# Performance work log

Measured on AMD Instinct MI355X. Metric: run time of the kernel, lower is better.

Reference implementation:

```python
import jax, jax.numpy as jnp
import numpy as np

B, D, S, U, H = 2, 1024, 2048, 1024, 16
LN_EPS = 1e-5

def setup_inputs() -> dict:
    key = jax.random.key(0)
    ks = jax.random.split(key, 5)
    std = 0.02
    return {
        "inputs": jax.random.normal(ks[0], (B, D, S), jnp.float32),
        "Wq": jax.random.normal(ks[1], (D, U), jnp.float32) * std,
        "bq": jnp.zeros((U,), jnp.float32),
        "Wk": jax.random.normal(ks[2], (D, U), jnp.float32) * std,
        "bk": jnp.zeros((U,), jnp.float32),
        "Wv": jax.random.normal(ks[3], (D, U), jnp.float32) * std,
        "bv": jnp.zeros((U,), jnp.float32),
        "Wo": jax.random.normal(ks[4], (U, D), jnp.float32) * std,
        "bo": jnp.zeros((D,), jnp.float32),
        "gamma": jnp.ones((D,), jnp.float32),
        "beta": jnp.zeros((D,), jnp.float32),
        "num_heads": H,
    }

def reference(inputs, Wq, bq, Wk, bk, Wv, bv, Wo, bo, gamma, beta, num_heads):
    # inputs: (B, D, S) -> (B, S, D)
    x = jnp.transpose(inputs, (0, 2, 1))
    b, s, d = x.shape

    def proj(W, bias):
        y = jax.nn.relu(x @ W + bias)               # (b, s, U)
        y = y.reshape(b, s, num_heads, -1)
        return jnp.transpose(y, (0, 2, 1, 3))       # (b, h, s, hd)

    Q = proj(Wq, bq)
    K = proj(Wk, bk)
    V = proj(Wv, bv)
    hd = Q.shape[-1]
    scale = 1.0 / np.sqrt(hd).astype(np.float32)

    # Block-wise flash attention in the source is mathematically plain softmax attention
    # (per-block epsilon 1e-10 is negligible); scale applied to Q, no mask, no dropout.
    scores = jnp.einsum('bhid,bhjd->bhij', Q * scale, K)   # (b, h, s, s)
    P = jax.nn.softmax(scores, axis=-1)
    O = jnp.einsum('bhij,bhjd->bhid', P, V)                # (b, h, s, hd)

    O = jnp.transpose(O, (0, 2, 1, 3)).reshape(b, s, -1)   # (b, s, U)
    out = O @ Wo + bo + x                                  # residual add
    mean = jnp.mean(out, axis=-1, keepdims=True)
    var = jnp.var(out, axis=-1, keepdims=True)
    y = (out - mean) * jax.lax.rsqrt(var + LN_EPS) * gamma + beta
    return jnp.transpose(y, (0, 2, 1))                     # (B, D, S)
```

## Files before the change

kernel.cpp:

```cpp
#include <hip/hip_runtime.h>
#include <hip/hip_bf16.h>

typedef __bf16 bf16x8 __attribute__((ext_vector_type(8)));
typedef __bf16 bf16x4 __attribute__((ext_vector_type(4)));
typedef float  f32x4  __attribute__((ext_vector_type(4)));
typedef float  f32x16 __attribute__((ext_vector_type(16)));

#define MFMA16(a, b, c) __builtin_amdgcn_mfma_f32_16x16x32_bf16((a), (b), (c), 0, 0, 0)
#define MFMA32(a, b, c) __builtin_amdgcn_mfma_f32_32x32x16_bf16((a), (b), (c), 0, 0, 0)

namespace {
constexpr int Bb = 2, Dd = 1024, Ss = 2048, Uu = 1024, Hh = 16;
}

#if __has_builtin(__builtin_amdgcn_exp2f)
#define EXP2(x) __builtin_amdgcn_exp2f(x)
#else
#define EXP2(x) __expf((x) * 0.6931471805599453f)
#endif

__device__ __forceinline__ uint32_t pkbf(float a, float b) {
  union { __bf16 h[2]; uint32_t u; } z;
  z.h[0] = (__bf16)a; z.h[1] = (__bf16)b;
  return z.u;
}
#define PLSWAP(a, b) asm("v_permlane32_swap_b32 %0, %1" : "+v"(a), "+v"(b))

__device__ __forceinline__ void gl16(const void* g, void* l) {
  __builtin_amdgcn_global_load_lds((const __attribute__((address_space(1))) uint32_t*)g,
                                   (__attribute__((address_space(3))) uint32_t*)l, 16, 0, 0);
}

#define VMW(n) asm volatile("s_waitcnt vmcnt(" #n ")" ::: "memory")
#define BARRIER_PIN() do { __builtin_amdgcn_s_barrier(); \
  asm volatile("" ::: "memory"); __builtin_amdgcn_sched_barrier(0); } while (0)
#define LGKM0() asm volatile("s_waitcnt lgkmcnt(0)" ::: "memory")

__global__ __launch_bounds__(256) void k_xpose_x(const float* __restrict__ inp,
                                                 __bf16* __restrict__ xb, float* __restrict__ xt) {
  __shared__ __attribute__((aligned(16))) float xs[64][65];
  const int s0 = blockIdx.x * 64, d0 = blockIdx.y * 64, b = blockIdx.z;
  const int t = threadIdx.x;
  {
    const int i = t >> 2, c = (t & 3) * 16;
    const float* src = inp + ((size_t)(b * Dd + d0 + i)) * Ss + s0 + c;
#pragma unroll
    for (int q = 0; q < 4; ++q) {
      const float4 f = *(const float4*)(src + q * 4);
      xs[i][c + q * 4 + 0] = f.x; xs[i][c + q * 4 + 1] = f.y;
      xs[i][c + q * 4 + 2] = f.z; xs[i][c + q * 4 + 3] = f.w;
    }
  }
  __syncthreads();
  {
    const int sl = t >> 2, dc = (t & 3) * 16;
    float* dstf = xt + ((size_t)(b * Ss + s0 + sl)) * Dd + d0 + dc;
    bf16x8 va, vb;
#pragma unroll
    for (int q = 0; q < 4; ++q) {
      float4 f;
      f.x = xs[dc + q * 4 + 0][sl]; f.y = xs[dc + q * 4 + 1][sl];
      f.z = xs[dc + q * 4 + 2][sl]; f.w = xs[dc + q * 4 + 3][sl];
      *(float4*)(dstf + q * 4) = f;
    }
#pragma unroll
    for (int j = 0; j < 8; ++j) { va[j] = (__bf16)xs[dc + j][sl]; vb[j] = (__bf16)xs[dc + 8 + j][sl]; }
    __bf16* dst = xb + ((size_t)(b * Ss + s0 + sl)) * Dd + d0 + dc;
    *(bf16x8*)dst = va;
    *(bf16x8*)(dst + 8) = vb;
  }
}

__global__ __launch_bounds__(256) void k_xpose_w(const float* __restrict__ w0, const float* __restrict__ w1,
                                                 const float* __restrict__ w2, const float* __restrict__ w3,
                                                 __bf16* __restrict__ o0, __bf16* __restrict__ o1,
                                                 __bf16* __restrict__ o2, __bf16* __restrict__ o3) {
  __shared__ __attribute__((aligned(16))) __bf16 ts[64][72];
  const float* src_m; __bf16* dst_m;
  switch (blockIdx.z) {
    case 0: src_m = w0; dst_m = o0; break;
    case 1: src_m = w1; dst_m = o1; break;
    case 2: src_m = w2; dst_m = o2; break;
    default: src_m = w3; dst_m = o3; break;
  }
  const int n0 = blockIdx.x * 64, k0 = blockIdx.y * 64;
  const int t = threadIdx.x;
  {
    const int i = t >> 2, c = (t & 3) * 16;
    const float* src = src_m + (size_t)(k0 + i) * 1024 + n0 + c;
#pragma unroll
    for (int q = 0; q < 4; ++q) {
      const float4 f = *(const float4*)(src + q * 4);
      ts[i][c + q * 4 + 0] = (__bf16)f.x;
      ts[i][c + q * 4 + 1] = (__bf16)f.y;
      ts[i][c + q * 4 + 2] = (__bf16)f.z;
      ts[i][c + q * 4 + 3] = (__bf16)f.w;
    }
  }
  __syncthreads();
  {
    const int nl = t >> 2, kc = (t & 3) * 16;
    bf16x8 va, vb;
#pragma unroll
    for (int j = 0; j < 8; ++j) { va[j] = ts[kc + j][nl]; vb[j] = ts[kc + 8 + j][nl]; }
    __bf16* dst = dst_m + (size_t)(n0 + nl) * 1024 + k0 + kc;
    *(bf16x8*)dst = va;
    *(bf16x8*)(dst + 8) = vb;
  }
}

__device__ __forceinline__ int swz_slot(int row, int slot) { return (slot + (row >> 1)) & 3; }

__device__ __forceinline__ void gemm_core(const __bf16* __restrict__ A, const __bf16* __restrict__ Bt,
                                          __bf16 (*__restrict__ As)[128][32], __bf16 (*__restrict__ Bs)[128][32],
                                          int m0, int n0, int t, f32x4 acc[4][4]) {
  const int w = t >> 6, l = t & 63;
  const int wm = (w >> 1) * 64, wn = (w & 1) * 64;
  const int lg = l >> 4, lr = l & 15;
  const int sr = t >> 2, sc8 = t & 3;
  const int so = ((sc8 + 4 - ((sr >> 1) & 3)) & 3) * 8;
  const __bf16* ga = A + (size_t)(m0 + sr) * 1024 + so;
  const __bf16* gb = Bt + (size_t)(n0 + sr) * 1024 + so;
  const int de = sr * 32 + sc8 * 8;
#define STG(bf, kk) { \
    gl16(ga + (kk) * 32,             &As[bf][0][0] + de); \
    gl16(ga + (kk) * 32 + 64 * 1024, &As[bf][0][0] + de + 64 * 32); \
    gl16(gb + (kk) * 32,             &Bs[bf][0][0] + de); \
    gl16(gb + (kk) * 32 + 64 * 1024, &Bs[bf][0][0] + de + 64 * 32); }
  STG(0, 0) STG(1, 1)
  for (int s = 0; s < 32; ++s) {
    if (s < 31) { VMW(4); } else { VMW(0); }
    BARRIER_PIN();
    if (s + 2 < 32) { const int b2 = (s + 2) % 3; STG(b2, s + 2) }
    const int cb = s % 3;
    bf16x8 af[4], bfr[4];
#pragma unroll
    for (int i = 0; i < 4; ++i) { const int rr = wm + i * 16 + lr; af[i]  = *(const bf16x8*)&As[cb][rr][swz_slot(rr, lg) * 8]; }
#pragma unroll
    for (int i = 0; i < 4; ++i) { const int rr = wn + i * 16 + lr; bfr[i] = *(const bf16x8*)&Bs[cb][rr][swz_slot(rr, lg) * 8]; }
#pragma unroll
    for (int i = 0; i < 4; ++i)
#pragma unroll
      for (int j = 0; j < 4; ++j) acc[i][j] = MFMA16(af[i], bfr[j], acc[i][j]);
  }
#undef STG
}

__device__ __forceinline__ void epi_qk_c(f32x4 acc[4][4], const float* bias, __bf16* out,
                                         int m0, int n0, int t, float scale, __bf16* Ct) {
  const int w = t >> 6, l = t & 63;
  const int wm = (w >> 1) * 64, wn = (w & 1) * 64;
  const int lg = l >> 4, lr = l & 15;
  __syncthreads();
#pragma unroll
  for (int j = 0; j < 4; ++j) {
    const int nl = wn + j * 16 + lr;
    const float bi = bias[n0 + nl];
#pragma unroll
    for (int i = 0; i < 4; ++i)
#pragma unroll
      for (int r = 0; r < 4; ++r) {
        const int ml = wm + i * 16 + lg * 4 + r;
        Ct[ml * 132 + nl] = (__bf16)(fmaxf(acc[i][j][r] + bi, 0.0f) * scale);
      }
  }
  __syncthreads();
  const int b = m0 >> 11, h0 = n0 >> 6, sb = m0 & 2047;
  const int sub = t & 7, rid0 = t >> 3;
#pragma unroll
  for (int p = 0; p < 8; ++p) {
    const int rid = p * 32 + rid0;
    const int sl = rid & 127, hh = rid >> 7;
    const bf16x8 v = *(const bf16x8*)&Ct[sl * 132 + hh * 64 + sub * 8];
    *(bf16x8*)(out + ((size_t)(b * Hh + h0 + hh) * Ss + sb + sl) * 64 + sub * 8) = v;
  }
}

__device__ __forceinline__ void epi_vt_c(f32x4 acc[4][4], const float* bias, __bf16* out,
                                         int m0, int n0, int t, __bf16* Ct) {
  const int w = t >> 6, l = t & 63;
  const int wm = (w >> 1) * 64, wn = (w & 1) * 64;
  const int lg = l >> 4, lr = l & 15;
  __syncthreads();
#pragma unroll
  for (int j = 0; j < 4; ++j) {
    const int nl = wn + j * 16 + lr;
    const float bi = bias[n0 + nl];
#pragma unroll
    for (int i = 0; i < 4; ++i)
#pragma unroll
      for (int r = 0; r < 4; ++r) {
        const int ml = wm + i * 16 + lg * 4 + r;
        Ct[nl * 132 + ml] = (__bf16)fmaxf(acc[i][j][r] + bi, 0.0f);
      }
  }
  __syncthreads();
  const int b = m0 >> 11, sb = m0 & 2047;
  const int sub = t & 15, rid0 = t >> 4;
#pragma unroll
  for (int p = 0; p < 8; ++p) {
    const int rid = p * 16 + rid0;
    const bf16x8 v = *(const bf16x8*)&Ct[rid * 132 + sub * 8];
    *(bf16x8*)(out + (size_t)(b * 1024 + n0 + rid) * Ss + sb + sub * 8) = v;
  }
}

__global__ __launch_bounds__(256) void k_gemm_qkv(const __bf16* __restrict__ A,
    const __bf16* __restrict__ W0, const __bf16* __restrict__ W1, const __bf16* __restrict__ W2,
    const float* __restrict__ b0, const float* __restrict__ b1, const float* __restrict__ b2,
    __bf16* __restrict__ Qb, __bf16* __restrict__ Kb, __bf16* __restrict__ Vt) {
  __shared__ __attribute__((aligned(16))) char smem[49152];
  auto As = (__bf16 (*)[128][32])smem;
  auto Bs = (__bf16 (*)[128][32])(smem + 24576);
  __bf16* Ct = (__bf16*)smem;
  const int flat = blockIdx.x;
  const int logical = (flat & 7) * 96 + (flat >> 3);
  const int z = logical >> 8;
  const int rem = logical & 255;
  const int n0 = (rem & 7) * 128, m0 = (rem >> 3) * 128;
  const __bf16* Bt = (z == 0) ? W0 : (z == 1) ? W1 : W2;
  const float* bias = (z == 0) ? b0 : (z == 1) ? b1 : b2;
  const int t = threadIdx.x;
  f32x4 acc[4][4] = {};
  gemm_core(A, Bt, As, Bs, m0, n0, t, acc);
  if (z == 0) epi_qk_c(acc, bias, Qb, m0, n0, t, 0.125f * 1.44269504f, Ct);
  else if (z == 1) epi_qk_c(acc, bias, Kb, m0, n0, t, 1.0f, Ct);
  else epi_vt_c(acc, bias, Vt, m0, n0, t, Ct);
}

__global__ __launch_bounds__(256) void k_gemm_o(const __bf16* __restrict__ A, const __bf16* __restrict__ Bt,
                                                const float* __restrict__ bias, const float* __restrict__ xt,
                                                float* __restrict__ Wb, float* __restrict__ partials) {
  __shared__ __attribute__((aligned(16))) char smem[49152];
  auto As = (__bf16 (*)[128][32])smem;
  auto Bs = (__bf16 (*)[128][32])(smem + 24576);
  float* Cs = (float*)smem;
  const int flat = blockIdx.x;
  const int logical = (flat & 7) * 32 + (flat >> 3);
  const int n0 = (logical & 7) * 128, m0 = (logical >> 3) * 128;
  const int t = threadIdx.x, w = t >> 6, l = t & 63;
  const int wm = (w >> 1) * 64, wn = (w & 1) * 64;
  const int lg = l >> 4, lr = l & 15;
  f32x4 acc[4][4] = {};
  gemm_core(A, Bt, As, Bs, m0, n0, t, acc);
  const int sub = t & 31, rid0 = t >> 5;
#pragma unroll
  for (int h2 = 0; h2 < 2; ++h2) {
    __syncthreads();
    if ((w >> 1) == h2) {
#pragma unroll
      for (int j = 0; j < 4; ++j) {
        const int nl = wn + j * 16 + lr;
        const float bi = bias[n0 + nl];
#pragma unroll
        for (int i = 0; i < 4; ++i)
#pragma unroll
          for (int r = 0; r < 4; ++r)
            Cs[(i * 16 + lg * 4 + r) * 132 + nl] = acc[i][j][r] + bi;
      }
    }
    __syncthreads();
#pragma unroll
    for (int p = 0; p < 8; ++p) {
      const int row = p * 8 + rid0;
      const int m = m0 + h2 * 64 + row;
      float4 v = *(const float4*)&Cs[row * 132 + sub * 4];
      const float4 x4 = *(const float4*)&xt[(size_t)m * 1024 + n0 + sub * 4];
      v.x += x4.x; v.y += x4.y; v.z += x4.z; v.w += x4.w;
      *(float4*)&Wb[(size_t)m * 1024 + n0 + sub * 4] = v;
      float s = v.x + v.y + v.z + v.w;
      float q = v.x * v.x + v.y * v.y + v.z * v.z + v.w * v.w;
      s += __shfl_xor(s, 1); s += __shfl_xor(s, 2); s += __shfl_xor(s, 4); s += __shfl_xor(s, 8);
      q += __shfl_xor(q, 1); q += __shfl_xor(q, 2); q += __shfl_xor(q, 4); q += __shfl_xor(q, 8);
      if ((sub & 15) == 0) {
        const int ci = (n0 >> 6) + (sub >> 4);
        partials[((size_t)m * 16 + ci) * 2]     = s;
        partials[((size_t)m * 16 + ci) * 2 + 1] = q;
      }
    }
  }
}

__global__ __launch_bounds__(256, 2) void k_attn6(const __bf16* __restrict__ Qg, const __bf16* __restrict__ Kg,
                                                  const __bf16* __restrict__ Vt, __bf16* __restrict__ Og) {
  __shared__ __attribute__((aligned(16))) char smem[36864];
  auto Ks = (__bf16 (*)[64][72])smem;
  auto Vs = (__bf16 (*)[64][72])(smem + 18432);
  __bf16* Os = (__bf16*)smem;
  const int t = threadIdx.x, l = t & 63, w = t >> 6;
  const int ln = l & 31, hi = l >> 5;
  const int bid = blockIdx.x;
  const int orig = (bid & 7) * 64 + (bid >> 3);
  const int bh = orig >> 4, qt = orig & 15;
  const int q0blk = qt * 128;
  const int q0w = q0blk + w * 32;
  const int b = bh >> 4, h = bh & 15;
  const size_t kbase = (size_t)bh * Ss * 64;
  const int srow = t >> 2, scol = (t & 3) * 16;
  const __bf16* Krow = Kg + kbase + (size_t)srow * 64 + scol;
  const __bf16* Vrow = Vt + (size_t)(bh * 64 + srow) * Ss + scol;

  bf16x8 qf0, qf1, qf2, qf3;
  {
    const __bf16* qp = Qg + kbase + (size_t)(q0w + ln) * 64 + hi * 8;
    qf0 = *(const bf16x8*)(qp);
    qf1 = *(const bf16x8*)(qp + 16);
    qf2 = *(const bf16x8*)(qp + 32);
    qf3 = *(const bf16x8*)(qp + 48);
  }
  f32x16 oA = {}, oB = {};
  float lrow = 0.f;

  auto tile_compute = [&](const __bf16 (&K)[64][72], const __bf16 (&V)[64][72]) {
    f32x16 s0 = {}, s1 = {};
    {
      bf16x8 kf;
#define QK(u, cc, sacc) \
      kf = *(const bf16x8*)&K[(u) * 32 + ln][(cc) * 16 + hi * 8]; \
      sacc = MFMA32(kf, qf##cc, sacc);
      QK(0, 0, s0) QK(0, 1, s0) QK(0, 2, s0) QK(0, 3, s0)
      QK(1, 0, s1) QK(1, 1, s1) QK(1, 2, s1) QK(1, 3, s1)
#undef QK
    }
#pragma unroll
    for (int r = 0; r < 16; ++r) s0[r] = EXP2(s0[r]);
#pragma unroll
    for (int r = 0; r < 16; ++r) s1[r] = EXP2(s1[r]);
    float sm[16];
#pragma unroll
    for (int r = 0; r < 8; ++r) sm[r] = s0[2 * r] + s0[2 * r + 1];
#pragma unroll
    for (int r = 0; r < 8; ++r) sm[8 + r] = s1[2 * r] + s1[2 * r + 1];
#pragma unroll
    for (int st = 8; st > 0; st >>= 1)
#pragma unroll
      for (int r = 0; r < st; ++r) sm[r] += sm[r + st];
    lrow += sm[0];
    uint32_t w0[8], w1[8];
#pragma unroll
    for (int k = 0; k < 8; ++k) w0[k] = pkbf(s0[2 * k], s0[2 * k + 1]);
#pragma unroll
    for (int k = 0; k < 8; ++k) w1[k] = pkbf(s1[2 * k], s1[2 * k + 1]);
    PLSWAP(w0[0], w0[2]); PLSWAP(w0[1], w0[3]);
    PLSWAP(w0[4], w0[6]); PLSWAP(w0[5], w0[7]);
    PLSWAP(w1[0], w1[2]); PLSWAP(w1[1], w1[3]);
    PLSWAP(w1[4], w1[6]); PLSWAP(w1[5], w1[7]);
    union U4 { uint32_t u[4]; bf16x8 v; };
    U4 z;
    bf16x8 pa0, pa1, pa2, pa3;
    z.u[0] = w0[0]; z.u[1] = w0[1]; z.u[2] = w0[2]; z.u[3] = w0[3]; pa0 = z.v;
    z.u[0] = w0[4]; z.u[1] = w0[5]; z.u[2] = w0[6]; z.u[3] = w0[7]; pa1 = z.v;
    z.u[0] = w1[0]; z.u[1] = w1[1]; z.u[2] = w1[2]; z.u[3] = w1[3]; pa2 = z.v;
    z.u[0] = w1[4]; z.u[1] = w1[5]; z.u[2] = w1[6]; z.u[3] = w1[7]; pa3 = z.v;
    {
      bf16x8 vf;
#define PV(half, ti, pa, oacc) \
      vf = *(const bf16x8*)&V[(half) * 32 + ln][(ti) * 16 + hi * 8]; \
      oacc = MFMA32(vf, pa, oacc);
      PV(0, 0, pa0, oA) PV(0, 1, pa1, oA) PV(0, 2, pa2, oA) PV(0, 3, pa3, oA)
      PV(1, 0, pa0, oB) PV(1, 1, pa1, oB) PV(1, 2, pa2, oB) PV(1, 3, pa3, oB)
#undef PV
    }
  };

  bf16x8 kA0 = *(const bf16x8*)(Krow),      kA1 = *(const bf16x8*)(Krow + 8);
  bf16x8 vA0 = *(const bf16x8*)(Vrow),      vA1 = *(const bf16x8*)(Vrow + 8);
  bf16x8 kB0 = *(const bf16x8*)(Krow + 64 * 64), kB1 = *(const bf16x8*)(Krow + 64 * 64 + 8);
  bf16x8 vB0 = *(const bf16x8*)(Vrow + 64), vB1 = *(const bf16x8*)(Vrow + 64 + 8);

  for (int tt = 0; tt < 16; ++tt) {
    *(bf16x8*)&Ks[0][srow][scol]     = kA0;
    *(bf16x8*)&Ks[0][srow][scol + 8] = kA1;
    *(bf16x8*)&Vs[0][srow][scol]     = vA0;
    *(bf16x8*)&Vs[0][srow][scol + 8] = vA1;
    LGKM0();
    BARRIER_PIN();
    if (tt < 15) {
      const size_t ko = (size_t)(2 * tt + 2) * 64;
      kA0 = *(const bf16x8*)(Krow + ko * 64);
      kA1 = *(const bf16x8*)(Krow + ko * 64 + 8);
      vA0 = *(const bf16x8*)(Vrow + ko);
      vA1 = *(const bf16x8*)(Vrow + ko + 8);
    }
    tile_compute(Ks[0], Vs[0]);
    *(bf16x8*)&Ks[1][srow][scol]     = kB0;
    *(bf16x8*)&Ks[1][srow][scol + 8] = kB1;
    *(bf16x8*)&Vs[1][srow][scol]     = vB0;
    *(bf16x8*)&Vs[1][srow][scol + 8] = vB1;
    LGKM0();
    BARRIER_PIN();
    if (tt < 15) {
      const size_t ko = (size_t)(2 * tt + 3) * 64;
      kB0 = *(const bf16x8*)(Krow + ko * 64);
      kB1 = *(const bf16x8*)(Krow + ko * 64 + 8);
      vB0 = *(const bf16x8*)(Vrow + ko);
      vB1 = *(const bf16x8*)(Vrow + ko + 8);
    }
    tile_compute(Ks[1], Vs[1]);
  }
  {
    uint32_t a = __builtin_bit_cast(uint32_t, lrow), bsw = a;
    PLSWAP(a, bsw);
    lrow = __builtin_bit_cast(float, a) + __builtin_bit_cast(float, bsw);
  }
  const float rl = 1.0f / lrow;
  __syncthreads();
  const int ql = w * 32 + ln;
#pragma unroll
  for (int r0 = 0; r0 < 4; ++r0)
#pragma unroll
    for (int j = 0; j < 4; ++j) {
      Os[ql * 68 + hi * 4 + r0 * 8 + j]      = (__bf16)(oA[r0 * 4 + j] * rl);
      Os[ql * 68 + 32 + hi * 4 + r0 * 8 + j] = (__bf16)(oB[r0 * 4 + j] * rl);
    }
  __syncthreads();
  const int sub = t & 7, rid0 = t >> 3;
#pragma unroll
  for (int p = 0; p < 4; ++p) {
    const int rid = p * 32 + rid0;
    const bf16x8 v = *(const bf16x8*)&Os[rid * 68 + sub * 8];
    *(bf16x8*)(Og + ((size_t)(b * Ss + q0blk + rid)) * Uu + h * 64 + sub * 8) = v;
  }
}

__global__ __launch_bounds__(256) void k_ln_stats(const float* __restrict__ partials, float* __restrict__ stats) {
  const int row = blockIdx.x * 256 + threadIdx.x;
  float s = 0.f, q = 0.f;
#pragma unroll
  for (int c = 0; c < 16; ++c) {
    s += partials[((size_t)row * 16 + c) * 2];
    q += partials[((size_t)row * 16 + c) * 2 + 1];
  }
  const float mean = s * (1.0f / 1024.0f);
  const float var = q * (1.0f / 1024.0f) - mean * mean;
  stats[row * 2] = mean;
  stats[row * 2 + 1] = rsqrtf(var + 1e-5f);
}

__global__ __launch_bounds__(256) void k_ln_write(const float* __restrict__ Wb, const float* __restrict__ stats,
                                                  const float* __restrict__ gamma, const float* __restrict__ beta,
                                                  float* __restrict__ out) {
  __shared__ __attribute__((aligned(16))) float ws0[64][65];
  __shared__ float sm[64][2];
  const int d0 = blockIdx.x * 64, s0 = blockIdx.y * 64, b = blockIdx.z;
  const int t = threadIdx.x;
  {
    const int sl = t >> 2, dc = (t & 3) * 16;
    const float* src = Wb + ((size_t)(b * Ss + s0 + sl)) * Dd + d0 + dc;
#pragma unroll
    for (int q = 0; q < 4; ++q) {
      const float4 f = *(const float4*)(src + q * 4);
      ws0[dc + q * 4 + 0][sl] = f.x; ws0[dc + q * 4 + 1][sl] = f.y;
      ws0[dc + q * 4 + 2][sl] = f.z; ws0[dc + q * 4 + 3][sl] = f.w;
    }
  }
  if (t < 128) sm[t >> 1][t & 1] = stats[(size_t)(b * Ss + s0 + (t >> 1)) * 2 + (t & 1)];
  __syncthreads();
  const int dl = t >> 2, sc = (t & 3) * 16;
  const float g = gamma[d0 + dl], be = beta[d0 + dl];
  float* dst = out + ((size_t)(b * Dd + d0 + dl)) * Ss + s0 + sc;
#pragma unroll
  for (int q = 0; q < 4; ++q) {
    float4 o;
    o.x = (ws0[dl][sc + q * 4 + 0] - sm[sc + q * 4 + 0][0]) * sm[sc + q * 4 + 0][1] * g + be;
    o.y = (ws0[dl][sc + q * 4 + 1] - sm[sc + q * 4 + 1][0]) * sm[sc + q * 4 + 1][1] * g + be;
    o.z = (ws0[dl][sc + q * 4 + 2] - sm[sc + q * 4 + 2][0]) * sm[sc + q * 4 + 2][1] * g + be;
    o.w = (ws0[dl][sc + q * 4 + 3] - sm[sc + q * 4 + 3][0]) * sm[sc + q * 4 + 3][1] * g + be;
    *(float4*)(dst + q * 4) = o;
  }
}

extern "C" void kernel_launch(void* const* d_in, const int* in_sizes, int n_in,
                              void* d_out, int out_size, void* d_ws, size_t ws_size,
                              hipStream_t stream) {
  const float* inp   = (const float*)d_in[0];
  const float* Wq    = (const float*)d_in[1];
  const float* bq    = (const float*)d_in[2];
  const float* Wk    = (const float*)d_in[3];
  const float* bk    = (const float*)d_in[4];
  const float* Wv    = (const float*)d_in[5];
  const float* bv    = (const float*)d_in[6];
  const float* Wo    = (const float*)d_in[7];
  const float* bo    = (const float*)d_in[8];
  const float* gamma = (const float*)d_in[9];
  const float* beta  = (const float*)d_in[10];

  char* ws = (char*)d_ws;
  const size_t MB = 1ull << 20;
  __bf16* xb  = (__bf16*)(ws);
  __bf16* Wqt = (__bf16*)(ws + 8 * MB);
  __bf16* Wkt = (__bf16*)(ws + 10 * MB);
  __bf16* Wvt = (__bf16*)(ws + 12 * MB);
  __bf16* Wot = (__bf16*)(ws + 14 * MB);
  __bf16* Qb  = (__bf16*)(ws + 16 * MB);
  __bf16* Kb  = (__bf16*)(ws + 24 * MB);
  __bf16* Vtb = (__bf16*)(ws + 32 * MB);
  __bf16* Ob  = (__bf16*)(ws + 40 * MB);
  float*  xt  = (float*)(ws + 48 * MB);
  float*  Wb  = (float*)(ws + 16 * MB);
  float*  partials = (float*)(ws + 8 * MB);
  float*  stats    = (float*)(ws + 8 * MB + 512 * 1024);

  k_xpose_x<<<dim3(32, 16, 2), 256, 0, stream>>>(inp, xb, xt);
  k_xpose_w<<<dim3(16, 16, 4), 256, 0, stream>>>(Wq, Wk, Wv, Wo, Wqt, Wkt, Wvt, Wot);
  k_gemm_qkv<<<dim3(768), 256, 0, stream>>>(xb, Wqt, Wkt, Wvt, bq, bk, bv, Qb, Kb, Vtb);
  k_attn6<<<dim3(512), 256, 0, stream>>>(Qb, Kb, Vtb, Ob);
  k_gemm_o<<<dim3(256), 256, 0, stream>>>(Ob, Wot, bo, xt, Wb, partials);
  k_ln_stats<<<dim3(16), 256, 0, stream>>>(partials, stats);
  k_ln_write<<<dim3(16, 32, 2), 256, 0, stream>>>(Wb, stats, gamma, beta, (float*)d_out);
}
```

Measured before the change: 145.4 us.

## Replace QKV GEMM with 256x256-tile, 8-wave, 4-stage pipelined kernel

The fused QKV projection GEMM now uses 256x256 output tiles with 512 threads (8 waves, each computing 128x64) instead of 128x128 tiles with 256 threads. It uses a 4-stage LDS ring with split A/B staging interleaved between two MFMA phases, setprio around MFMA bursts, and a chunked epilogue that writes Q/K head-major and V transposed via LDS. The aim is more operand reuse per LDS load and less global traffic per FLOP. In exchange the grid shrinks from 768 to 192 blocks, fewer than the CU count, and register and LDS pressure rise.

```diff
diff --git a/kernel.cpp b/kernel.cpp
--- a/kernel.cpp
+++ b/kernel.cpp
@@ -106,6 +106,147 @@
     __bf16* dst = dst_m + (size_t)(n0 + nl) * 1024 + k0 + kc;
     *(bf16x8*)dst = va;
     *(bf16x8*)(dst + 8) = vb;
+  }
+}
+
+__global__ __launch_bounds__(512, 2) void k_gemm_qkv8(const __bf16* __restrict__ A,
+    const __bf16* __restrict__ W0, const __bf16* __restrict__ W1, const __bf16* __restrict__ W2,
+    const float* __restrict__ b0, const float* __restrict__ b1, const float* __restrict__ b2,
+    __bf16* __restrict__ Qb, __bf16* __restrict__ Kb, __bf16* __restrict__ Vt) {
+  __shared__ __attribute__((aligned(16))) __bf16 As[4][256][32];
+  __shared__ __attribute__((aligned(16))) __bf16 Bs[4][256][32];
+  const int t = threadIdx.x;
+  const int w = t >> 6, l = t & 63, lg = l >> 4, lr = l & 15;
+  const int wm = w >> 2, wn = w & 3;
+  const int bid = blockIdx.x;
+  const int logical = (bid & 7) * 24 + (bid >> 3);
+  const int z = logical >> 6;
+  const int rem = logical & 63;
+  const int n0 = (rem & 3) * 256, m0 = (rem >> 2) * 256;
+  const __bf16* Bt = z == 0 ? W0 : z == 1 ? W1 : W2;
+  const float* bias = z == 0 ? b0 : z == 1 ? b1 : b2;
+
+  const int srow = t >> 2, scol = (t & 3) * 8;
+  const __bf16* gaB = A  + ((size_t)(m0 + srow)) * 1024 + scol;
+  const __bf16* gbB = Bt + ((size_t)(n0 + srow)) * 1024 + scol;
+#define STG_A(s, h, kt) gl16(gaB + (size_t)(h) * 128 * 1024 + (kt) * 32, &As[s][(h) * 128 + srow][scol])
+#define STG_B(s, h, kt) gl16(gbB + (size_t)(h) * 128 * 1024 + (kt) * 32, &Bs[s][(h) * 128 + srow][scol])
+
+  STG_A(0, 0, 0); STG_A(0, 1, 0); STG_B(0, 0, 0); STG_B(0, 1, 0);
+  STG_A(1, 0, 1); STG_A(1, 1, 1); STG_B(1, 0, 1); STG_B(1, 1, 1);
+  STG_A(2, 0, 2); STG_A(2, 1, 2); STG_B(2, 0, 2); STG_B(2, 1, 2);
+  f32x4 acc[8][4] = {};
+  VMW(8);
+  BARRIER_PIN();
+
+  const __bf16* Abase = &As[0][0][0] + wm * 4096 + lr * 32 + lg * 8;
+  const __bf16* Bbase = &Bs[0][0][0] + wn * 2048 + lr * 32 + lg * 8;
+
+  for (int kt = 0; kt < 32; ++kt) {
+    const int sC = kt & 3, sS = (kt + 3) & 3;
+    const __bf16* Ap = Abase + sC * 8192;
+    const __bf16* Bp = Bbase + sC * 8192;
+    bf16x8 a0, a1, a2, a3, bb0, bb1, bb2, bb3;
+    a0 = *(const bf16x8*)(Ap);         a1 = *(const bf16x8*)(Ap + 512);
+    a2 = *(const bf16x8*)(Ap + 1024);  a3 = *(const bf16x8*)(Ap + 1536);
+    bb0 = *(const bf16x8*)(Bp);        bb1 = *(const bf16x8*)(Bp + 512);
+    bb2 = *(const bf16x8*)(Bp + 1024); bb3 = *(const bf16x8*)(Bp + 1536);
+    if (kt < 29) { STG_A(sS, 0, kt + 3); STG_A(sS, 1, kt + 3); }
+    BARRIER_PIN();
+    LGKM0(); __builtin_amdgcn_sched_barrier(0);
+    __builtin_amdgcn_s_setprio(1);
+    acc[0][0] = MFMA16(a0, bb0, acc[0][0]); acc[0][1] = MFMA16(a0, bb1, acc[0][1]);
+    acc[0][2] = MFMA16(a0, bb2, acc[0][2]); acc[0][3] = MFMA16(a0, bb3, acc[0][3]);
+    acc[1][0] = MFMA16(a1, bb0, acc[1][0]); acc[1][1] = MFMA16(a1, bb1, acc[1][1]);
+    acc[1][2] = MFMA16(a1, bb2, acc[1][2]); acc[1][3] = MFMA16(a1, bb3, acc[1][3]);
+    acc[2][0] = MFMA16(a2, bb0, acc[2][0]); acc[2][1] = MFMA16(a2, bb1, acc[2][1]);
+    acc[2][2] = MFMA16(a2, bb2, acc[2][2]); acc[2][3] = MFMA16(a2, bb3, acc[2][3]);
+    acc[3][0] = MFMA16(a3, bb0, acc[3][0]); acc[3][1] = MFMA16(a3, bb1, acc[3][1]);
+    acc[3][2] = MFMA16(a3, bb2, acc[3][2]); acc[3][3] = MFMA16(a3, bb3, acc[3][3]);
+    __builtin_amdgcn_s_setprio(0);
+    BARRIER_PIN();
+    a0 = *(const bf16x8*)(Ap + 2048);  a1 = *(const bf16x8*)(Ap + 2560);
+    a2 = *(const bf16x8*)(Ap + 3072);  a3 = *(const bf16x8*)(Ap + 3584);
+    if (kt < 29) { STG_B(sS, 0, kt + 3); STG_B(sS, 1, kt + 3); }
+    if (kt < 29) { VMW(8); } else if (kt == 29) { VMW(4); } else if (kt == 30) { VMW(0); }
+    BARRIER_PIN();
+    LGKM0(); __builtin_amdgcn_sched_barrier(0);
+    __builtin_amdgcn_s_setprio(1);
+    acc[4][0] = MFMA16(a0, bb0, acc[4][0]); acc[4][1] = MFMA16(a0, bb1, acc[4][1]);
+    acc[4][2] = MFMA16(a0, bb2, acc[4][2]); acc[4][3] = MFMA16(a0, bb3, acc[4][3]);
+    acc[5][0] = MFMA16(a1, bb0, acc[5][0]); acc[5][1] = MFMA16(a1, bb1, acc[5][1]);
+    acc[5][2] = MFMA16(a1, bb2, acc[5][2]); acc[5][3] = MFMA16(a1, bb3, acc[5][3]);
+    acc[6][0] = MFMA16(a2, bb0, acc[6][0]); acc[6][1] = MFMA16(a2, bb1, acc[6][1]);
+    acc[6][2] = MFMA16(a2, bb2, acc[6][2]); acc[6][3] = MFMA16(a2, bb3, acc[6][3]);
+    acc[7][0] = MFMA16(a3, bb0, acc[7][0]); acc[7][1] = MFMA16(a3, bb1, acc[7][1]);
+    acc[7][2] = MFMA16(a3, bb2, acc[7][2]); acc[7][3] = MFMA16(a3, bb3, acc[7][3]);
+    __builtin_amdgcn_s_setprio(0);
+    BARRIER_PIN();
+  }
+#undef STG_A
+#undef STG_B
+
+  const int b = m0 >> 11, sb = m0 & 2047;
+  __bf16* Ct = &As[0][0][0];
+  float bi[4];
+#pragma unroll
+  for (int j = 0; j < 4; ++j) bi[j] = bias[n0 + wn * 64 + j * 16 + lr];
+  if (z < 2) {
+    __bf16* out = z == 0 ? Qb : Kb;
+    const float scale = z == 0 ? 0.125f * 1.44269504f : 1.0f;
+    const int h0 = n0 >> 6;
+    for (int c = 0; c < 4; ++c) {
+      __syncthreads();
+      if (wm == (c >> 1)) {
+        const int q = c & 1;
+#pragma unroll
+        for (int j = 0; j < 4; ++j) {
+          const int nl = wn * 64 + j * 16 + lr;
+#pragma unroll
+          for (int i2 = 0; i2 < 4; ++i2)
+#pragma unroll
+            for (int r = 0; r < 4; ++r)
+              Ct[(i2 * 16 + lg * 4 + r) * 264 + nl] =
+                  (__bf16)(fmaxf(acc[q * 4 + i2][j][r] + bi[j], 0.0f) * scale);
+        }
+      }
+      __syncthreads();
+#pragma unroll
+      for (int u4 = 0; u4 < 4; ++u4) {
+        const int u = u4 * 512 + t;
+        const int sl = u >> 5, ru = u & 31;
+        const int hh = ru >> 3, sg = ru & 7;
+        const bf16x8 v = *(const bf16x8*)&Ct[sl * 264 + hh * 64 + sg * 8];
+        *(bf16x8*)(out + ((size_t)(b * Hh + h0 + hh) * Ss + sb + c * 64 + sl) * 64 + sg * 8) = v;
+      }
+    }
+  } else {
+    for (int c = 0; c < 4; ++c) {
+      __syncthreads();
+      if (wn == c) {
+#pragma unroll
+        for (int j = 0; j < 4; ++j) {
+          const int nli = j * 16 + lr;
+#pragma unroll
+          for (int mi = 0; mi < 8; ++mi)
+#pragma unroll
+            for (int r2 = 0; r2 < 4; r2 += 2) {
+              const int ml = wm * 128 + mi * 16 + lg * 4 + r2;
+              const uint32_t pk = pkbf(fmaxf(acc[mi][j][r2] + bi[j], 0.0f),
+                                       fmaxf(acc[mi][j][r2 + 1] + bi[j], 0.0f));
+              *(uint32_t*)&Ct[nli * 264 + ml] = pk;
+            }
+        }
+      }
+      __syncthreads();
+#pragma unroll
+      for (int u4 = 0; u4 < 4; ++u4) {
+        const int u = u4 * 512 + t;
+        const int nl = u >> 5, sg = u & 31;
+        const bf16x8 v = *(const bf16x8*)&Ct[nl * 264 + sg * 8];
+        *(bf16x8*)(Vt + (size_t)(b * 1024 + n0 + c * 64 + nl) * Ss + sb + sg * 8) = v;
+      }
+    }
   }
 }
 
@@ -144,88 +285,6 @@
       for (int j = 0; j < 4; ++j) acc[i][j] = MFMA16(af[i], bfr[j], acc[i][j]);
   }
 #undef STG
-}
-
-__device__ __forceinline__ void epi_qk_c(f32x4 acc[4][4], const float* bias, __bf16* out,
-                                         int m0, int n0, int t, float scale, __bf16* Ct) {
-  const int w = t >> 6, l = t & 63;
-  const int wm = (w >> 1) * 64, wn = (w & 1) * 64;
-  const int lg = l >> 4, lr = l & 15;
-  __syncthreads();
-#pragma unroll
-  for (int j = 0; j < 4; ++j) {
-    const int nl = wn + j * 16 + lr;
-    const float bi = bias[n0 + nl];
-#pragma unroll
-    for (int i = 0; i < 4; ++i)
-#pragma unroll
-      for (int r = 0; r < 4; ++r) {
-        const int ml = wm + i * 16 + lg * 4 + r;
-        Ct[ml * 132 + nl] = (__bf16)(fmaxf(acc[i][j][r] + bi, 0.0f) * scale);
-      }
-  }
-  __syncthreads();
-  const int b = m0 >> 11, h0 = n0 >> 6, sb = m0 & 2047;
-  const int sub = t & 7, rid0 = t >> 3;
-#pragma unroll
-  for (int p = 0; p < 8; ++p) {
-    const int rid = p * 32 + rid0;
-    const int sl = rid & 127, hh = rid >> 7;
-    const bf16x8 v = *(const bf16x8*)&Ct[sl * 132 + hh * 64 + sub * 8];
-    *(bf16x8*)(out + ((size_t)(b * Hh + h0 + hh) * Ss + sb + sl) * 64 + sub * 8) = v;
-  }
-}
-
-__device__ __forceinline__ void epi_vt_c(f32x4 acc[4][4], const float* bias, __bf16* out,
-                                         int m0, int n0, int t, __bf16* Ct) {
-  const int w = t >> 6, l = t & 63;
-  const int wm = (w >> 1) * 64, wn = (w & 1) * 64;
-  const int lg = l >> 4, lr = l & 15;
-  __syncthreads();
-#pragma unroll
-  for (int j = 0; j < 4; ++j) {
-    const int nl = wn + j * 16 + lr;
-    const float bi = bias[n0 + nl];
-#pragma unroll
-    for (int i = 0; i < 4; ++i)
-#pragma unroll
-      for (int r = 0; r < 4; ++r) {
-        const int ml = wm + i * 16 + lg * 4 + r;
-        Ct[nl * 132 + ml] = (__bf16)fmaxf(acc[i][j][r] + bi, 0.0f);
-      }
-  }
-  __syncthreads();
-  const int b = m0 >> 11, sb = m0 & 2047;
-  const int sub = t & 15, rid0 = t >> 4;
-#pragma unroll
-  for (int p = 0; p < 8; ++p) {
-    const int rid = p * 16 + rid0;
-    const bf16x8 v = *(const bf16x8*)&Ct[rid * 132 + sub * 8];
-    *(bf16x8*)(out + (size_t)(b * 1024 + n0 + rid) * Ss + sb + sub * 8) = v;
-  }
-}
-
-__global__ __launch_bounds__(256) void k_gemm_qkv(const __bf16* __restrict__ A,
-    const __bf16* __restrict__ W0, const __bf16* __restrict__ W1, const __bf16* __restrict__ W2,
-    const float* __restrict__ b0, const float* __restrict__ b1, const float* __restrict__ b2,
-    __bf16* __restrict__ Qb, __bf16* __restrict__ Kb, __bf16* __restrict__ Vt) {
-  __shared__ __attribute__((aligned(16))) char smem[49152];
-  auto As = (__bf16 (*)[128][32])smem;
-  auto Bs = (__bf16 (*)[128][32])(smem + 24576);
-  __bf16* Ct = (__bf16*)smem;
-  const int flat = blockIdx.x;
-  const int logical = (flat & 7) * 96 + (flat >> 3);
-  const int z = logical >> 8;
-  const int rem = logical & 255;
-  const int n0 = (rem & 7) * 128, m0 = (rem >> 3) * 128;
-  const __bf16* Bt = (z == 0) ? W0 : (z == 1) ? W1 : W2;
-  const float* bias = (z == 0) ? b0 : (z == 1) ? b1 : b2;
-  const int t = threadIdx.x;
-  f32x4 acc[4][4] = {};
-  gemm_core(A, Bt, As, Bs, m0, n0, t, acc);
-  if (z == 0) epi_qk_c(acc, bias, Qb, m0, n0, t, 0.125f * 1.44269504f, Ct);
-  else if (z == 1) epi_qk_c(acc, bias, Kb, m0, n0, t, 1.0f, Ct);
-  else epi_vt_c(acc, bias, Vt, m0, n0, t, Ct);
 }
 
 __global__ __launch_bounds__(256) void k_gemm_o(const __bf16* __restrict__ A, const __bf16* __restrict__ Bt,
@@ -503,7 +562,7 @@
 
   k_xpose_x<<<dim3(32, 16, 2), 256, 0, stream>>>(inp, xb, xt);
   k_xpose_w<<<dim3(16, 16, 4), 256, 0, stream>>>(Wq, Wk, Wv, Wo, Wqt, Wkt, Wvt, Wot);
-  k_gemm_qkv<<<dim3(768), 256, 0, stream>>>(xb, Wqt, Wkt, Wvt, bq, bk, bv, Qb, Kb, Vtb);
+  k_gemm_qkv8<<<dim3(192), 512, 0, stream>>>(xb, Wqt, Wkt, Wvt, bq, bk, bv, Qb, Kb, Vtb);
   k_attn6<<<dim3(512), 256, 0, stream>>>(Qb, Kb, Vtb, Ob);
   k_gemm_o<<<dim3(256), 256, 0, stream>>>(Ob, Wot, bo, xt, Wb, partials);
   k_ln_stats<<<dim3(16), 256, 0, stream>>>(partials, stats);
```

Result: no change. 143.0 us (-1.6%).
